# Optimization experiments

Measured on AMD Instinct MI355X. Metric: run time of the kernel, lower is better.

The kernel has to match this reference:

```python
import jax, jax.numpy as jnp
import numpy as np

IN_CH = 256
MED_CH = IN_CH // 2


def setup_inputs() -> dict:
    key = jax.random.key(0)
    ks = jax.random.split(key, 9)
    B, C, H, W = 16, IN_CH, 64, 64
    s = 1.0 / np.sqrt(C)
    sm = 1.0 / np.sqrt(MED_CH)
    return {
        "x": jax.random.normal(ks[0], (B, C, H, W), dtype=jnp.float32),
        "w_o": jax.random.normal(ks[1], (MED_CH, C), dtype=jnp.float32) * s,
        "b_o": jax.random.normal(ks[2], (MED_CH,), dtype=jnp.float32) * 0.01,
        "w_v": jax.random.normal(ks[3], (MED_CH, C), dtype=jnp.float32) * s,
        "b_v": jax.random.normal(ks[4], (MED_CH,), dtype=jnp.float32) * 0.01,
        "w_c": jax.random.normal(ks[5], (C, MED_CH), dtype=jnp.float32) * sm,
        "b_c": jax.random.normal(ks[6], (C,), dtype=jnp.float32) * 0.01,
        "gamma": jax.random.normal(ks[7], (1,), dtype=jnp.float32) * 0.1,
    }


def reference(x, w_o, b_o, w_v, b_v, w_c, b_c, gamma):
    B, C, H, W = x.shape
    N = H * W
    xf = x.reshape(B, C, N)  # [B,C,N]
    # 1x1 convs == per-pixel linear projections
    o = jnp.einsum("mc,bcn->bmn", w_o, xf) + b_o[None, :, None]   # [B,M,N]
    v = jnp.einsum("mc,bcn->bmn", w_v, xf) + b_v[None, :, None]   # [B,M,N]
    x_o = o.transpose(0, 2, 1)                                     # [B,N,M]
    x_v = jax.nn.softmax(v, axis=-1)                               # softmax over N
    # NOTE: original code reuses conv_v for the 's' branch (conv_s unused)
    x_s = jax.nn.softmax(v.transpose(0, 2, 1), axis=-1)            # [B,N,M], softmax over M
    A = jnp.einsum("bmn,bnk->bmk", x_v, x_s)                       # [B,M,M]
    Bt = jnp.einsum("bnm,bmk->bnk", x_o, A).transpose(0, 2, 1)     # [B,M,N]
    out = jax.nn.relu(jnp.einsum("cm,bmn->bcn", w_c, Bt) + b_c[None, :, None])
    result = gamma[0] * out.reshape(B, C, H, W) + x
    return result
```

## Files before the change

kernel.cpp:

```cpp
#include <hip/hip_runtime.h>
#include <math.h>

constexpr int Bn = 16;
constexpr int Cn = 256;
constexpr int Mn = 128;
constexpr int Nn = 4096;

typedef short bf16x8 __attribute__((ext_vector_type(8)));
typedef float f32x4 __attribute__((ext_vector_type(4)));
typedef unsigned short us8 __attribute__((ext_vector_type(8)));
typedef unsigned short us4 __attribute__((ext_vector_type(4)));

static __device__ __forceinline__ unsigned short f2bf(float f) {
  union { float f; unsigned int u; } c{f};
  unsigned int u = c.u;
  u += 0x7FFFu + ((u >> 16) & 1u);
  return (unsigned short)(u >> 16);
}

static __device__ __forceinline__ void gload_lds16(const void* g, void* l) {
  __builtin_amdgcn_global_load_lds(
      (const __attribute__((address_space(1))) unsigned int*)g,
      (__attribute__((address_space(3))) unsigned int*)l, 16, 0, 0);
}

__global__ __launch_bounds__(256) void k_prep(
    const float* __restrict__ x, unsigned short* __restrict__ xT,
    const float* __restrict__ w_o, const float* __restrict__ w_v,
    unsigned short* __restrict__ Wv, unsigned short* __restrict__ woT,
    float* __restrict__ rs) {
  const int b = blockIdx.z;
  const int c0 = blockIdx.y * 128;
  const int n0 = blockIdx.x * 64;
  const int t = threadIdx.x;

  if (blockIdx.y == 0 && blockIdx.z == 0) {
    int idx = blockIdx.x * 256 + t;
    if (idx < Bn * Mn) rs[idx] = 0.f;
    if (idx < 8192) {
      int row = idx >> 6;
      int c4 = (idx & 63) * 4;
      float4 f = *(const float4*)&w_v[(size_t)row * Cn + c4];
      us4 g = {f2bf(f.x), f2bf(f.y), f2bf(f.z), f2bf(f.w)};
      *(us4*)&Wv[(size_t)row * Cn + c4] = g;
    } else {
      int j = idx - 8192;
      int cp = j >> 5;
      int m4 = (j & 31) * 4;
      us4 g;
#pragma unroll
      for (int e = 0; e < 4; ++e) g[e] = f2bf(w_o[(size_t)(m4 + e) * Cn + cp]);
      *(us4*)&woT[(size_t)cp * Mn + m4] = g;
    }
  }

  const int n4 = (t & 15) * 4;
  const int c8 = c0 + (t >> 4) * 8;
  const float* xb = x + ((size_t)b * Cn + c8) * Nn + n0 + n4;
  float4 r[8];
#pragma unroll
  for (int i = 0; i < 8; ++i) r[i] = *(const float4*)&xb[(size_t)i * Nn];
  unsigned short* dst = xT + ((size_t)b * Nn + n0 + n4) * Cn + c8;
#pragma unroll
  for (int j = 0; j < 4; ++j) {
    us8 g;
#pragma unroll
    for (int i = 0; i < 8; ++i) g[i] = f2bf(((const float*)&r[i])[j]);
    *(us8*)&dst[(size_t)j * Cn] = g;
  }
}

__global__ __launch_bounds__(256) void k_proj_v(
    const unsigned short* __restrict__ Wv,
    const unsigned short* __restrict__ xT,
    const float* __restrict__ b_v,
    float* __restrict__ Ap, float* __restrict__ rs) {
  __shared__ us8 pool[2 * 8 * 128];
  __shared__ float cs_lds[2][64];
  unsigned short* ldsA = (unsigned short*)pool;
  unsigned short* ldsB = (unsigned short*)pool + 8 * 128 * 8;
  const int b = blockIdx.y;
  const int nt = blockIdx.x;
  const int t = threadIdx.x;
  const int wave = t >> 6, lane = t & 63;
  const int quad = lane >> 4, l16 = lane & 15;
  const int wm = (wave & 1) * 64;
  const int wn = (wave >> 1) * 32;
  const int wk = (wave >> 1) * 64;
  f32x4 acc[4][4] = {};
  const unsigned short* xb = xT + ((size_t)b * Nn + nt * 64) * Cn;

  uint4 rB[2];
#pragma unroll
  for (int p = 0; p < 2; ++p) {
    int s = p * 256 + t;
    rB[p] = *(const uint4*)&xb[(size_t)(s & 63) * Cn + (s >> 6) * 8];
  }

  for (int k0 = 0; k0 < Cn; k0 += 64) {
#pragma unroll
    for (int p = 0; p < 2; ++p) {
      int s = p * 256 + t;
      *(uint4*)&ldsB[(size_t)s * 8] = rB[p];
    }
#pragma unroll
    for (int p = 0; p < 4; ++p) {
      int s = p * 256 + t;
      gload_lds16(&Wv[(size_t)(s & 127) * Cn + k0 + (s >> 7) * 8],
                  &ldsA[(size_t)s * 8]);
    }
    __syncthreads();
    if (k0 + 64 < Cn) {
#pragma unroll
      for (int p = 0; p < 2; ++p) {
        int s = p * 256 + t;
        rB[p] = *(const uint4*)&xb[(size_t)(s & 63) * Cn + k0 + 64 + (s >> 6) * 8];
      }
    }
#pragma unroll
    for (int ss = 0; ss < 2; ++ss) {
      int g4 = ss * 4 + quad;
      bf16x8 af[4], bfr[2];
#pragma unroll
      for (int i = 0; i < 4; ++i)
        af[i] = *(const bf16x8*)&ldsA[(size_t)(g4 * 128 + wm + i * 16 + l16) * 8];
#pragma unroll
      for (int j = 0; j < 2; ++j)
        bfr[j] = *(const bf16x8*)&ldsB[(size_t)(g4 * 64 + wn + j * 16 + l16) * 8];
#pragma unroll
      for (int i = 0; i < 4; ++i)
#pragma unroll
        for (int j = 0; j < 2; ++j)
          acc[i][j] = __builtin_amdgcn_mfma_f32_16x16x32_bf16(af[i], bfr[j], acc[i][j], 0, 0, 0);
    }
    __syncthreads();
  }

#pragma unroll
  for (int i = 0; i < 4; ++i) {
#pragma unroll
    for (int r = 0; r < 4; ++r) {
      float bi = b_v[wm + i * 16 + quad * 4 + r];
#pragma unroll
      for (int j = 0; j < 2; ++j)
        acc[i][j][r] = __expf(acc[i][j][r] + bi);
    }
  }

#pragma unroll
  for (int i = 0; i < 4; ++i) {
#pragma unroll
    for (int r = 0; r < 4; ++r) {
      float s = acc[i][0][r] + acc[i][1][r];
      s += __shfl_xor(s, 1); s += __shfl_xor(s, 2);
      s += __shfl_xor(s, 4); s += __shfl_xor(s, 8);
      if (l16 == 0)
        atomicAdd(&rs[b * Mn + wm + i * 16 + quad * 4 + r], s);
    }
  }

  float csj[2];
#pragma unroll
  for (int j = 0; j < 2; ++j) {
    float c = 0.f;
#pragma unroll
    for (int i = 0; i < 4; ++i)
#pragma unroll
      for (int r = 0; r < 4; ++r) c += acc[i][j][r];
    c += __shfl_xor(c, 16);
    c += __shfl_xor(c, 32);
    csj[j] = c;
  }
  if (quad == 0) {
#pragma unroll
    for (int j = 0; j < 2; ++j) cs_lds[wave & 1][wn + j * 16 + l16] = csj[j];
  }
  __syncthreads();

  float rinv[2];
#pragma unroll
  for (int j = 0; j < 2; ++j) {
    int nl = wn + j * 16 + l16;
    rinv[j] = rsqrtf(cs_lds[0][nl] + cs_lds[1][nl]);
  }

  unsigned short* Hs = (unsigned short*)pool;
  unsigned short* Ls = Hs + 8 * 128 * 8;
#pragma unroll
  for (int i = 0; i < 4; ++i) {
#pragma unroll
    for (int r = 0; r < 4; ++r) {
      int m = wm + i * 16 + quad * 4 + r;
#pragma unroll
      for (int j = 0; j < 2; ++j) {
        int nl = wn + j * 16 + l16;
        float u = acc[i][j][r] * rinv[j];
        unsigned short h = f2bf(u);
        union { unsigned int q; float f; } hf{(unsigned int)h << 16};
        int idx = ((nl >> 3) * 128 + (m ^ (nl >> 3))) * 8 + (nl & 7);
        Hs[idx] = h;
        Ls[idx] = f2bf(u - hf.f);
      }
    }
  }
  __syncthreads();

  const bf16x8* Hv = (const bf16x8*)pool;
  const bf16x8* Lv = Hv + 8 * 128;
#pragma unroll
  for (int i = 0; i < 4; ++i)
#pragma unroll
    for (int j = 0; j < 4; ++j) acc[i][j] = (f32x4){0.f, 0.f, 0.f, 0.f};
#pragma unroll
  for (int ss = 0; ss < 2; ++ss) {
    int g = ss * 4 + quad;
    bf16x8 hA[4], lA[4], hB[4], lB[4];
#pragma unroll
    for (int i = 0; i < 4; ++i) {
      int mi = wm + i * 16 + l16;
      int ki = wk + i * 16 + l16;
      hA[i] = Hv[g * 128 + (mi ^ g)];
      lA[i] = Lv[g * 128 + (mi ^ g)];
      hB[i] = Hv[g * 128 + (ki ^ g)];
      lB[i] = Lv[g * 128 + (ki ^ g)];
    }
#pragma unroll
    for (int i = 0; i < 4; ++i)
#pragma unroll
      for (int j = 0; j < 4; ++j) {
        acc[i][j] = __builtin_amdgcn_mfma_f32_16x16x32_bf16(hA[i], hB[j], acc[i][j], 0, 0, 0);
        acc[i][j] = __builtin_amdgcn_mfma_f32_16x16x32_bf16(hA[i], lB[j], acc[i][j], 0, 0, 0);
        acc[i][j] = __builtin_amdgcn_mfma_f32_16x16x32_bf16(lA[i], hB[j], acc[i][j], 0, 0, 0);
      }
  }

  float* Apb = Ap + ((size_t)nt * Bn + b) * (Mn * Mn);
#pragma unroll
  for (int i = 0; i < 4; ++i) {
#pragma unroll
    for (int r = 0; r < 4; ++r) {
      int m = wm + i * 16 + quad * 4 + r;
      float* row = &Apb[(size_t)m * Mn];
#pragma unroll
      for (int j = 0; j < 4; ++j)
        row[wk + j * 16 + l16] = acc[i][j][r];
    }
  }
}

__global__ __launch_bounds__(256) void k_reduceA(
    const float* __restrict__ Ap, const float* __restrict__ rs,
    float* __restrict__ A, int S) {
  int tid = blockIdx.x * 256 + threadIdx.x;
  int idx4 = tid * 4;
  int b = idx4 / (Mn * Mn);
  int off = idx4 - b * (Mn * Mn);
  float4 s = {0.f, 0.f, 0.f, 0.f};
  for (int s0 = 0; s0 < S; ++s0) {
    float4 p = *(const float4*)&Ap[((size_t)s0 * Bn + b) * (Mn * Mn) + off];
    s.x += p.x; s.y += p.y; s.z += p.z; s.w += p.w;
  }
  float sc = 1.0f / rs[b * Mn + (off >> 7)];
  s.x *= sc; s.y *= sc; s.z *= sc; s.w *= sc;
  *(float4*)&A[idx4] = s;
}

__global__ __launch_bounds__(256) void k_w2(
    const float* __restrict__ w_c, const float* __restrict__ A,
    unsigned short* __restrict__ W2bf) {
  __shared__ float As[64][68];
  __shared__ float wcs[64][68];
  const int b = blockIdx.z;
  const int m0 = blockIdx.x * 64;
  const int c0 = blockIdx.y * 64;
  const int t = threadIdx.x;
  const int tc = (t >> 4) * 4, tmm = (t & 15) * 4;
  float acc[4][4] = {};
  for (int k0 = 0; k0 < Mn; k0 += 64) {
    int r = t >> 2;
    int k4 = (t & 3) * 4;
#pragma unroll
    for (int p = 0; p < 4; ++p) {
      int k = k4 + p * 16;
      float4 a4 = *(const float4*)&A[((size_t)(b * Mn + m0 + r)) * Mn + k0 + k];
      As[k + 0][r] = a4.x; As[k + 1][r] = a4.y; As[k + 2][r] = a4.z; As[k + 3][r] = a4.w;
      float4 w4 = *(const float4*)&w_c[(size_t)(c0 + r) * Mn + k0 + k];
      wcs[k + 0][r] = w4.x; wcs[k + 1][r] = w4.y; wcs[k + 2][r] = w4.z; wcs[k + 3][r] = w4.w;
    }
    __syncthreads();
#pragma unroll
    for (int kk = 0; kk < 64; ++kk) {
      float4 w4 = *(const float4*)&wcs[kk][tc];
      float4 a4 = *(const float4*)&As[kk][tmm];
      float w[4] = {w4.x, w4.y, w4.z, w4.w};
      float a[4] = {a4.x, a4.y, a4.z, a4.w};
#pragma unroll
      for (int i = 0; i < 4; ++i)
#pragma unroll
        for (int jj = 0; jj < 4; ++jj) acc[i][jj] = fmaf(w[i], a[jj], acc[i][jj]);
    }
    __syncthreads();
  }
#pragma unroll
  for (int i = 0; i < 4; ++i) {
    us4 g4 = {f2bf(acc[i][0]), f2bf(acc[i][1]), f2bf(acc[i][2]), f2bf(acc[i][3])};
    *(us4*)&W2bf[((size_t)(b * Cn + c0 + tc + i)) * Mn + m0 + tmm] = g4;
  }
}

__global__ __launch_bounds__(256) void k_ww(
    const unsigned short* __restrict__ W2bf, const unsigned short* __restrict__ woT,
    const float* __restrict__ b_o, const float* __restrict__ b_c,
    unsigned short* __restrict__ WW, float* __restrict__ bb) {
  __shared__ us8 ldsA[128 * 16];
  __shared__ us8 ldsB[128 * 16];
  __shared__ float bo_lds[128];
  const int b = blockIdx.z;
  const int c_t = blockIdx.y * 128;
  const int cp_t = blockIdx.x * 128;
  const int t = threadIdx.x;
  const int wave = t >> 6, lane = t & 63;
  const int quad = lane >> 4, l16 = lane & 15;
  const int wc = (wave & 1) * 64, wp = (wave >> 1) * 64;
  const unsigned short* W2b = W2bf + ((size_t)b * Cn + c_t) * Mn;
  const unsigned short* woB = woT + (size_t)cp_t * Mn;

#pragma unroll
  for (int p = 0; p < 8; ++p) {
    int s = p * 256 + t;
    int row = s >> 4, g = s & 15;
    int slot = row * 16 + (g ^ (row & 15));
    ldsA[slot] = *(const us8*)&W2b[(size_t)row * Mn + g * 8];
    ldsB[slot] = *(const us8*)&woB[(size_t)row * Mn + g * 8];
  }
  if (blockIdx.x == 0 && t < 128) bo_lds[t] = b_o[t];
  __syncthreads();

  f32x4 acc[4][4] = {};
#pragma unroll
  for (int s = 0; s < 4; ++s) {
    int gq = s * 4 + quad;
    int xo = gq ^ l16;
    bf16x8 af[4], bfr[4];
#pragma unroll
    for (int i = 0; i < 4; ++i)
      af[i] = *(const bf16x8*)&ldsA[(wc + i * 16 + l16) * 16 + xo];
#pragma unroll
    for (int j = 0; j < 4; ++j)
      bfr[j] = *(const bf16x8*)&ldsB[(wp + j * 16 + l16) * 16 + xo];
#pragma unroll
    for (int i = 0; i < 4; ++i)
#pragma unroll
      for (int j = 0; j < 4; ++j)
        acc[i][j] = __builtin_amdgcn_mfma_f32_16x16x32_bf16(af[i], bfr[j], acc[i][j], 0, 0, 0);
  }

#pragma unroll
  for (int i = 0; i < 4; ++i) {
#pragma unroll
    for (int r = 0; r < 4; ++r) {
      int c = c_t + wc + i * 16 + quad * 4 + r;
      unsigned short* row = &WW[((size_t)b * Cn + c) * Cn + cp_t];
#pragma unroll
      for (int j = 0; j < 4; ++j)
        row[wp + j * 16 + l16] = f2bf(acc[i][j][r]);
    }
  }

  if (blockIdx.x == 0 && t < 128) {
    float s = 0.f;
#pragma unroll
    for (int g = 0; g < 16; ++g) {
      us8 h = ldsA[t * 16 + (g ^ (t & 15))];
#pragma unroll
      for (int e = 0; e < 8; ++e) {
        union { unsigned int u; float f; } cv{(unsigned int)h[e] << 16};
        s = fmaf(cv.f, bo_lds[g * 8 + e], s);
      }
    }
    bb[b * Cn + c_t + t] = s + b_c[c_t + t];
  }
}

__global__ __launch_bounds__(256) void k_final_mfma(
    const unsigned short* __restrict__ WW, const unsigned short* __restrict__ xT,
    const float* __restrict__ x, const float* __restrict__ bb,
    const float* __restrict__ gamma, float* __restrict__ out) {
  __shared__ us8 ldsA[128 * 16];
  __shared__ us8 ldsB[128 * 16];
  const int flat = blockIdx.x + 32 * blockIdx.y + 64 * (int)blockIdx.z;
  const int swz = (flat & 7) * 128 + (flat >> 3);
  const int n_t = (swz & 31) * 128;
  const int c_t = ((swz >> 5) & 1) * 128;
  const int b = swz >> 6;
  const int t = threadIdx.x;
  const int wave = t >> 6, lane = t & 63;
  const int quad = lane >> 4, l16 = lane & 15;
  const int wc = (wave & 1) * 64, wn = (wave >> 1) * 64;
  const unsigned short* WWb = WW + ((size_t)b * Cn + c_t) * Cn;
  const unsigned short* xTb = xT + ((size_t)b * Nn + n_t) * Cn;
  unsigned short* ldsAu = (unsigned short*)ldsA;
  unsigned short* ldsBu = (unsigned short*)ldsB;

  f32x4 acc[4][4] = {};
  for (int k0 = 0; k0 < Cn; k0 += 128) {
#pragma unroll
    for (int p = 0; p < 8; ++p) {
      int s = p * 256 + t;
      int row = s >> 4, g = s & 15;
      int gsw = g ^ (row & 15);
      gload_lds16(&WWb[(size_t)row * Cn + k0 + gsw * 8], &ldsAu[(size_t)s * 8]);
      gload_lds16(&xTb[(size_t)row * Cn + k0 + gsw * 8], &ldsBu[(size_t)s * 8]);
    }
    __syncthreads();
#pragma unroll
    for (int s = 0; s < 4; ++s) {
      int gq = s * 4 + quad;
      int xo = gq ^ l16;
      bf16x8 af[4], bfr[4];
#pragma unroll
      for (int i = 0; i < 4; ++i)
        af[i] = *(const bf16x8*)&ldsA[(wc + i * 16 + l16) * 16 + xo];
#pragma unroll
      for (int j = 0; j < 4; ++j)
        bfr[j] = *(const bf16x8*)&ldsB[(wn + j * 16 + l16) * 16 + xo];
#pragma unroll
      for (int i = 0; i < 4; ++i)
#pragma unroll
        for (int j = 0; j < 4; ++j)
          acc[i][j] = __builtin_amdgcn_mfma_f32_16x16x32_bf16(af[i], bfr[j], acc[i][j], 0, 0, 0);
    }
    __syncthreads();
  }

  float g = gamma[0];
#pragma unroll
  for (int i = 0; i < 4; ++i) {
#pragma unroll
    for (int r = 0; r < 4; ++r) {
      int c = c_t + wc + i * 16 + quad * 4 + r;
      float bias = bb[b * Cn + c];
      const float* xr = &x[((size_t)b * Cn + c) * Nn + n_t];
      float* orow = &out[((size_t)b * Cn + c) * Nn + n_t];
#pragma unroll
      for (int j = 0; j < 4; ++j) {
        int n = wn + j * 16 + l16;
        orow[n] = g * fmaxf(acc[i][j][r] + bias, 0.f) + xr[n];
      }
    }
  }
}

extern "C" void kernel_launch(void* const* d_in, const int* in_sizes, int n_in,
                              void* d_out, int out_size, void* d_ws, size_t ws_size,
                              hipStream_t stream) {
  const float* x   = (const float*)d_in[0];
  const float* w_o = (const float*)d_in[1];
  const float* b_o = (const float*)d_in[2];
  const float* w_v = (const float*)d_in[3];
  const float* b_v = (const float*)d_in[4];
  const float* w_c = (const float*)d_in[5];
  const float* b_c = (const float*)d_in[6];
  const float* gm  = (const float*)d_in[7];

  constexpr int S = Nn / 64;
  float* ws = (float*)d_ws;
  float* rs = ws;
  float* bb = rs + Bn * Mn;
  float* A  = bb + Bn * Cn;
  float* Ap = A + (size_t)Bn * Mn * Mn;
  unsigned short* WW   = (unsigned short*)(Ap + (size_t)S * Bn * Mn * Mn);
  unsigned short* W2bf = WW + (size_t)Bn * Cn * Cn;
  unsigned short* xT   = W2bf + (size_t)Bn * Cn * Mn;
  unsigned short* Wv   = xT + (size_t)Bn * Nn * Cn;
  unsigned short* woT  = Wv + (size_t)Mn * Cn;

  k_prep<<<dim3(Nn / 64, 2, Bn), 256, 0, stream>>>(x, xT, w_o, w_v, Wv, woT, rs);
  k_proj_v<<<dim3(Nn / 64, Bn), 256, 0, stream>>>(Wv, xT, b_v, Ap, rs);
  k_reduceA<<<dim3(Bn * Mn * Mn / 1024), 256, 0, stream>>>(Ap, rs, A, S);
  k_w2<<<dim3(Mn / 64, Cn / 64, Bn), 256, 0, stream>>>(w_c, A, W2bf);
  k_ww<<<dim3(2, 2, Bn), 256, 0, stream>>>(W2bf, woT, b_o, b_c, WW, bb);
  k_final_mfma<<<dim3(Nn / 128, Cn / 128, Bn), 256, 0, stream>>>(WW, xT, x, bb, gm, (float*)d_out);
}
```

Baseline: 233.5 us.

## Double the proj_v N-tile to 128 with 512 threads and double-buffered LDS

k_proj_v now handles 128 pixels per block with 8 waves, which halves the number of partial A matrices written to global memory and later summed by k_reduceA. The K loop is fully unrolled with double-buffered LDS for both the weight and the activation tiles, so the next tile loads while the current one is computed. The cost is more LDS per block, fewer blocks (grid of 32x16), and a longer per-block reduction over 128 pixels in the second MFMA stage.

```diff
diff --git a/kernel.cpp b/kernel.cpp
--- a/kernel.cpp
+++ b/kernel.cpp
@@ -70,51 +70,52 @@
   }
 }
 
-__global__ __launch_bounds__(256) void k_proj_v(
+__global__ __launch_bounds__(512, 4) void k_proj_v(
     const unsigned short* __restrict__ Wv,
     const unsigned short* __restrict__ xT,
     const float* __restrict__ b_v,
     float* __restrict__ Ap, float* __restrict__ rs) {
-  __shared__ us8 pool[2 * 8 * 128];
-  __shared__ float cs_lds[2][64];
-  unsigned short* ldsA = (unsigned short*)pool;
-  unsigned short* ldsB = (unsigned short*)pool + 8 * 128 * 8;
+  __shared__ us8 pool[4][8 * 128];
+  __shared__ float cs_lds[2][128];
   const int b = blockIdx.y;
   const int nt = blockIdx.x;
   const int t = threadIdx.x;
   const int wave = t >> 6, lane = t & 63;
   const int quad = lane >> 4, l16 = lane & 15;
   const int wm = (wave & 1) * 64;
-  const int wn = (wave >> 1) * 32;
-  const int wk = (wave >> 1) * 64;
-  f32x4 acc[4][4] = {};
-  const unsigned short* xb = xT + ((size_t)b * Nn + nt * 64) * Cn;
+  const int wq = wave >> 1;
+  const int wn = wq * 32;
+  f32x4 acc[4][2] = {};
+  const unsigned short* xb = xT + ((size_t)b * Nn + nt * 128) * Cn;
 
   uint4 rB[2];
 #pragma unroll
   for (int p = 0; p < 2; ++p) {
-    int s = p * 256 + t;
-    rB[p] = *(const uint4*)&xb[(size_t)(s & 63) * Cn + (s >> 6) * 8];
-  }
-
-  for (int k0 = 0; k0 < Cn; k0 += 64) {
-#pragma unroll
-    for (int p = 0; p < 2; ++p) {
-      int s = p * 256 + t;
-      *(uint4*)&ldsB[(size_t)s * 8] = rB[p];
-    }
-#pragma unroll
-    for (int p = 0; p < 4; ++p) {
-      int s = p * 256 + t;
-      gload_lds16(&Wv[(size_t)(s & 127) * Cn + k0 + (s >> 7) * 8],
-                  &ldsA[(size_t)s * 8]);
-    }
-    __syncthreads();
-    if (k0 + 64 < Cn) {
+    int s = p * 512 + t;
+    rB[p] = *(const uint4*)&xb[(size_t)(s & 127) * Cn + (s >> 7) * 8];
+    gload_lds16(&Wv[(size_t)(s & 127) * Cn + (s >> 7) * 8],
+                &((unsigned short*)pool[0])[(size_t)s * 8]);
+  }
+#pragma unroll
+  for (int p = 0; p < 2; ++p) {
+    int s = p * 512 + t;
+    *(uint4*)&((unsigned short*)pool[2])[(size_t)s * 8] = rB[p];
+  }
+  __syncthreads();
+
+#pragma unroll
+  for (int tt = 0; tt < 4; ++tt) {
+    const int cur = tt & 1;
+    unsigned short* bufAc = (unsigned short*)pool[cur];
+    unsigned short* bufBc = (unsigned short*)pool[2 + cur];
+    if (tt < 3) {
+      int k1 = (tt + 1) * 64;
 #pragma unroll
       for (int p = 0; p < 2; ++p) {
-        int s = p * 256 + t;
-        rB[p] = *(const uint4*)&xb[(size_t)(s & 63) * Cn + k0 + 64 + (s >> 6) * 8];
+        int s = p * 512 + t;
+        rB[p] = *(const uint4*)&xb[(size_t)(s & 127) * Cn + k1 + (s >> 7) * 8];
+        gload_lds16(&Wv[(size_t)(s & 127) * Cn + k1 + (s >> 7) * 8],
+                    &((unsigned short*)pool[cur ^ 1])[(size_t)s * 8]);
       }
     }
 #pragma unroll
@@ -123,15 +124,22 @@
       bf16x8 af[4], bfr[2];
 #pragma unroll
       for (int i = 0; i < 4; ++i)
-        af[i] = *(const bf16x8*)&ldsA[(size_t)(g4 * 128 + wm + i * 16 + l16) * 8];
+        af[i] = *(const bf16x8*)&bufAc[(size_t)(g4 * 128 + wm + i * 16 + l16) * 8];
 #pragma unroll
       for (int j = 0; j < 2; ++j)
-        bfr[j] = *(const bf16x8*)&ldsB[(size_t)(g4 * 64 + wn + j * 16 + l16) * 8];
+        bfr[j] = *(const bf16x8*)&bufBc[(size_t)(g4 * 128 + wn + j * 16 + l16) * 8];
 #pragma unroll
       for (int i = 0; i < 4; ++i)
 #pragma unroll
         for (int j = 0; j < 2; ++j)
           acc[i][j] = __builtin_amdgcn_mfma_f32_16x16x32_bf16(af[i], bfr[j], acc[i][j], 0, 0, 0);
+    }
+    if (tt < 3) {
+#pragma unroll
+      for (int p = 0; p < 2; ++p) {
+        int s = p * 512 + t;
+        *(uint4*)&((unsigned short*)pool[2 + (cur ^ 1)])[(size_t)s * 8] = rB[p];
+      }
     }
     __syncthreads();
   }
@@ -185,7 +193,7 @@
   }
 
   unsigned short* Hs = (unsigned short*)pool;
-  unsigned short* Ls = Hs + 8 * 128 * 8;
+  unsigned short* Ls = Hs + 16 * 128 * 8;
 #pragma unroll
   for (int i = 0; i < 4; ++i) {
 #pragma unroll
@@ -206,28 +214,32 @@
   __syncthreads();
 
   const bf16x8* Hv = (const bf16x8*)pool;
-  const bf16x8* Lv = Hv + 8 * 128;
+  const bf16x8* Lv = Hv + 16 * 128;
+  const int wk = wq * 32;
 #pragma unroll
   for (int i = 0; i < 4; ++i)
 #pragma unroll
-    for (int j = 0; j < 4; ++j) acc[i][j] = (f32x4){0.f, 0.f, 0.f, 0.f};
-#pragma unroll
-  for (int ss = 0; ss < 2; ++ss) {
-    int g = ss * 4 + quad;
-    bf16x8 hA[4], lA[4], hB[4], lB[4];
+    for (int j = 0; j < 2; ++j) acc[i][j] = (f32x4){0.f, 0.f, 0.f, 0.f};
+#pragma unroll
+  for (int sg = 0; sg < 4; ++sg) {
+    int g = sg * 4 + quad;
+    bf16x8 hA[4], lA[4], hB[2], lB[2];
 #pragma unroll
     for (int i = 0; i < 4; ++i) {
       int mi = wm + i * 16 + l16;
-      int ki = wk + i * 16 + l16;
       hA[i] = Hv[g * 128 + (mi ^ g)];
       lA[i] = Lv[g * 128 + (mi ^ g)];
-      hB[i] = Hv[g * 128 + (ki ^ g)];
-      lB[i] = Lv[g * 128 + (ki ^ g)];
+    }
+#pragma unroll
+    for (int j = 0; j < 2; ++j) {
+      int ki = wk + j * 16 + l16;
+      hB[j] = Hv[g * 128 + (ki ^ g)];
+      lB[j] = Lv[g * 128 + (ki ^ g)];
     }
 #pragma unroll
     for (int i = 0; i < 4; ++i)
 #pragma unroll
-      for (int j = 0; j < 4; ++j) {
+      for (int j = 0; j < 2; ++j) {
         acc[i][j] = __builtin_amdgcn_mfma_f32_16x16x32_bf16(hA[i], hB[j], acc[i][j], 0, 0, 0);
         acc[i][j] = __builtin_amdgcn_mfma_f32_16x16x32_bf16(hA[i], lB[j], acc[i][j], 0, 0, 0);
         acc[i][j] = __builtin_amdgcn_mfma_f32_16x16x32_bf16(lA[i], hB[j], acc[i][j], 0, 0, 0);
@@ -242,7 +254,7 @@
       int m = wm + i * 16 + quad * 4 + r;
       float* row = &Apb[(size_t)m * Mn];
 #pragma unroll
-      for (int j = 0; j < 4; ++j)
+      for (int j = 0; j < 2; ++j)
         row[wk + j * 16 + l16] = acc[i][j][r];
     }
   }
@@ -463,7 +475,7 @@
   const float* b_c = (const float*)d_in[6];
   const float* gm  = (const float*)d_in[7];
 
-  constexpr int S = Nn / 64;
+  constexpr int S = Nn / 128;
   float* ws = (float*)d_ws;
   float* rs = ws;
   float* bb = rs + Bn * Mn;
@@ -476,7 +488,7 @@
   unsigned short* woT  = Wv + (size_t)Mn * Cn;
 
   k_prep<<<dim3(Nn / 64, 2, Bn), 256, 0, stream>>>(x, xT, w_o, w_v, Wv, woT, rs);
-  k_proj_v<<<dim3(Nn / 64, Bn), 256, 0, stream>>>(Wv, xT, b_v, Ap, rs);
+  k_proj_v<<<dim3(Nn / 128, Bn), 512, 0, stream>>>(Wv, xT, b_v, Ap, rs);
   k_reduceA<<<dim3(Bn * Mn * Mn / 1024), 256, 0, stream>>>(Ap, rs, A, S);
   k_w2<<<dim3(Mn / 64, Cn / 64, Bn), 256, 0, stream>>>(w_c, A, W2bf);
   k_ww<<<dim3(2, 2, Bn), 256, 0, stream>>>(W2bf, woT, b_o, b_c, WW, bb);
```

Result: faster. 203.0 us (-13.1%).
